# Optimization experiments

Measured on AMD Instinct MI355X. Metric: run time of the kernel, lower is better.

The kernel has to match this reference:

```python
import jax, jax.numpy as jnp
import numpy as np

H = 16      # attention_head_num
DH = 64     # attention_head_size
D = H * DH  # out_dim = 1024


def setup_inputs() -> dict:
    key = jax.random.key(0)
    ks = jax.random.split(key, 9)
    s = 1.0 / np.sqrt(D)
    x = jax.random.normal(ks[0], (2, 2048, D), dtype=jnp.float32)
    Wq = jax.random.uniform(ks[1], (D, D), jnp.float32, -s, s)
    bq = jax.random.uniform(ks[2], (D,), jnp.float32, -s, s)
    Wk = jax.random.uniform(ks[3], (D, D), jnp.float32, -s, s)
    bk = jax.random.uniform(ks[4], (D,), jnp.float32, -s, s)
    Wv = jax.random.uniform(ks[5], (D, D), jnp.float32, -s, s)
    bv = jax.random.uniform(ks[6], (D,), jnp.float32, -s, s)
    Wo = jax.random.uniform(ks[7], (D, D), jnp.float32, -s, s)
    bo = jax.random.uniform(ks[8], (D,), jnp.float32, -s, s)
    return {"x": x, "Wq": Wq, "bq": bq, "Wk": Wk, "bk": bk,
            "Wv": Wv, "bv": bv, "Wo": Wo, "bo": bo}


def reference(x, Wq, bq, Wk, bk, Wv, bv, Wo, bo):
    B, S, _ = x.shape
    # projections (nn.Linear: x @ W^T + b)
    q = (x @ Wq.T + bq).reshape(B, S, H, DH).transpose(0, 2, 1, 3)  # [B,H,S,Dh]
    k = (x @ Wk.T + bk).reshape(B, S, H, DH).transpose(0, 2, 1, 3)
    v = (x @ Wv.T + bv).reshape(B, S, H, DH).transpose(0, 2, 1, 3)
    scores = jnp.einsum('bhqd,bhkd->bhqk', q, k) / jnp.sqrt(jnp.float32(DH))
    probs = jax.nn.softmax(scores, axis=-1)  # dropout is identity in eval mode
    ctx = jnp.einsum('bhqk,bhkd->bhqd', probs, v)
    ctx = ctx.transpose(0, 2, 1, 3).reshape(B, S, D)
    return ctx @ Wo.T + bo
```

## Files before the change

kernel.cpp:

```cpp
#include <hip/hip_runtime.h>
#include <hip/hip_bf16.h>
#include <stdint.h>

typedef __attribute__((ext_vector_type(8))) short bf16x8;
typedef __attribute__((ext_vector_type(8))) unsigned short u16x8;
typedef __attribute__((ext_vector_type(4))) unsigned short u16x4;
typedef __attribute__((ext_vector_type(4))) float f32x4;

constexpr int NB  = 2;
constexpr int NS  = 2048;
constexpr int NH  = 16;
constexpr int NDH = 64;
constexpr int ND  = 1024;

static __device__ __forceinline__ unsigned short bfbits(float f) {
    union { float f; uint32_t u; } v; v.f = f;
    uint32_t u = v.u + 0x7FFFu + ((v.u >> 16) & 1u);
    return (unsigned short)(u >> 16);
}

static __device__ __forceinline__ float fexp2(float x) {
#if __has_builtin(__builtin_amdgcn_exp2f)
    return __builtin_amdgcn_exp2f(x);
#else
    return exp2f(x);
#endif
}

static __device__ __forceinline__ void gl_lds16(const void* g, void* l) {
    __builtin_amdgcn_global_load_lds(
        (const __attribute__((address_space(1))) unsigned int*)g,
        (__attribute__((address_space(3))) unsigned int*)l, 16, 0, 0);
}

__global__ __launch_bounds__(256)
void cvt_kernel(const float* __restrict__ x,  const float* __restrict__ wq,
                const float* __restrict__ wk, const float* __restrict__ wv,
                const float* __restrict__ wo,
                unsigned short* __restrict__ xb,  unsigned short* __restrict__ wqb,
                unsigned short* __restrict__ wkb, unsigned short* __restrict__ wvb,
                unsigned short* __restrict__ wob)
{
    const int b = blockIdx.x;
    const float* s; unsigned short* d; int off;
    if      (b < 2048) { s = x;  d = xb;  off = b; }
    else if (b < 2560) { s = wq; d = wqb; off = b - 2048; }
    else if (b < 3072) { s = wk; d = wkb; off = b - 2560; }
    else if (b < 3584) { s = wv; d = wvb; off = b - 3072; }
    else               { s = wo; d = wob; off = b - 3584; }
    const size_t idx = ((size_t)off * 256 + threadIdx.x) * 8;
    float4 f0 = *(const float4*)&s[idx];
    float4 f1 = *(const float4*)&s[idx + 4];
    u16x8 o;
    o[0] = bfbits(f0.x); o[1] = bfbits(f0.y); o[2] = bfbits(f0.z); o[3] = bfbits(f0.w);
    o[4] = bfbits(f1.x); o[5] = bfbits(f1.y); o[6] = bfbits(f1.z); o[7] = bfbits(f1.w);
    *(u16x8*)&d[idx] = o;
}

__global__ __launch_bounds__(256, 2)
void qkv_kernel(const unsigned short* __restrict__ xb,
                const unsigned short* __restrict__ wqb,
                const unsigned short* __restrict__ wkb,
                const unsigned short* __restrict__ wvb,
                const float* __restrict__ bq, const float* __restrict__ bk,
                const float* __restrict__ bv,
                unsigned short* __restrict__ qbuf,
                unsigned short* __restrict__ kbuf,
                unsigned short* __restrict__ vtbuf)
{
    __shared__ unsigned short As[128 * 64];
    __shared__ unsigned short Bs[128 * 64];
    __shared__ unsigned short Tt[128][136];

    const int fid = blockIdx.x + blockIdx.y * 24;
    const int xcd = fid & 7, idx = fid >> 3;
    const int bx  = idx >> 2;
    const int by  = xcd * 4 + (idx & 3);

    const int m0  = by * 128;
    const int jg0 = bx * 128;
    const int proj = jg0 >> 10;
    const int n0   = jg0 & 1023;
    const unsigned short* W = (proj == 0) ? wqb : (proj == 1) ? wkb : wvb;
    const float* bias       = (proj == 0) ? bq  : (proj == 1) ? bk  : bv;

    const int tid = threadIdx.x, lane = tid & 63, wid = tid >> 6;
    const int wm = wid >> 1, wn = wid & 1;
    const int l15 = lane & 15, g = lane >> 4;

    const f32x4 fzero = {0.f, 0.f, 0.f, 0.f};
    f32x4 acc[4][4];
#pragma unroll
    for (int i = 0; i < 4; i++)
#pragma unroll
        for (int j = 0; j < 4; j++) acc[i][j] = fzero;

    const int srow = tid >> 3;
    const int scb  = ((tid & 7) * 16) ^ ((srow & 7) << 4);
    const char* asrc = (const char*)xb + (size_t)(m0 + srow) * 2048 + scb;
    const char* bsrc = (const char*)W  + (size_t)(n0 + srow) * 2048 + scb;
    char* adst = (char*)As + tid * 16;
    char* bdst = (char*)Bs + tid * 16;
    const int xm = (l15 & 7) << 4;

    for (int k0 = 0; k0 < 1024; k0 += 64) {
#pragma unroll
        for (int i = 0; i < 4; i++) {
            gl_lds16(asrc + (size_t)i * 32 * 2048 + k0 * 2, adst + i * 4096);
            gl_lds16(bsrc + (size_t)i * 32 * 2048 + k0 * 2, bdst + i * 4096);
        }
        __syncthreads();
#pragma unroll
        for (int kk = 0; kk < 2; kk++) {
            bf16x8 af[4], bfr[4];
#pragma unroll
            for (int i = 0; i < 4; i++) {
                const int row = wm * 64 + i * 16 + l15;
                af[i] = *(const bf16x8*)((const char*)As + row * 128 + ((kk * 64 + g * 16) ^ xm));
            }
#pragma unroll
            for (int j = 0; j < 4; j++) {
                const int row = wn * 64 + j * 16 + l15;
                bfr[j] = *(const bf16x8*)((const char*)Bs + row * 128 + ((kk * 64 + g * 16) ^ xm));
            }
#pragma unroll
            for (int i = 0; i < 4; i++)
#pragma unroll
                for (int j = 0; j < 4; j++)
                    acc[i][j] = __builtin_amdgcn_mfma_f32_16x16x32_bf16(af[i], bfr[j], acc[i][j], 0, 0, 0);
        }
        __syncthreads();
    }

    if (proj < 2) {
        unsigned short* qk_out = (proj == 0) ? qbuf : kbuf;
        const float qs = (proj == 0) ? 0.18033688f : 1.0f;
#pragma unroll
        for (int j = 0; j < 4; j++) {
            const int col = n0 + wn * 64 + j * 16 + l15;
            const float bsv = bias[col];
            const int h = col >> 6, dh = col & 63;
#pragma unroll
            for (int i = 0; i < 4; i++)
#pragma unroll
                for (int r = 0; r < 4; r++) {
                    const int row = m0 + wm * 64 + i * 16 + g * 4 + r;
                    const int b_ = row >> 11, s_ = row & (NS - 1);
                    qk_out[((size_t)((b_ * NH + h) * NS + s_)) * NDH + dh] =
                        bfbits((acc[i][j][r] + bsv) * qs);
                }
        }
    } else {
#pragma unroll
        for (int j = 0; j < 4; j++) {
            const int cl = wn * 64 + j * 16 + l15;
            const float bsv = bias[n0 + cl];
#pragma unroll
            for (int i = 0; i < 4; i++) {
                u16x4 w4;
#pragma unroll
                for (int r = 0; r < 4; r++) w4[r] = bfbits(acc[i][j][r] + bsv);
                *(u16x4*)&Tt[cl][wm * 64 + i * 16 + g * 4] = w4;
            }
        }
        __syncthreads();
        const int b_ = m0 >> 11, s0 = m0 & (NS - 1);
        const int h0 = n0 >> 6;
#pragma unroll
        for (int it = 0; it < 8; it++) {
            const int c = wid * 32 + it * 4 + g;
            u16x8 v8 = *(const u16x8*)&Tt[c][l15 * 8];
            const size_t row = (size_t)(b_ * NH + h0 + (c >> 6)) * NDH + (c & 63);
            *(u16x8*)&vtbuf[row * NS + s0 + l15 * 8] = v8;
        }
    }
}

__global__ __launch_bounds__(512, 4)
void attn_kernel(const unsigned short* __restrict__ qbuf,
                 const unsigned short* __restrict__ kbuf,
                 const unsigned short* __restrict__ vtbuf,
                 unsigned short* __restrict__ ctxbuf)
{
    __shared__ unsigned short Ks[2][128 * 64];
    __shared__ unsigned short Vs[2][64 * 128];

    const int fid  = blockIdx.x + blockIdx.y * 16;
    const int nid  = (fid % 8) * 64 + fid / 8;
    const int bx   = nid % 16, bh = nid / 16;
    const int q0   = bx * 128;

    const int tid = threadIdx.x, lane = tid & 63, wid = tid >> 6;
    const int l15 = lane & 15, g = lane >> 4;

    const unsigned short* qb = qbuf  + (size_t)bh * NS * NDH;
    const unsigned short* kb = kbuf  + (size_t)bh * NS * NDH;
    const unsigned short* vb = vtbuf + (size_t)bh * NDH * NS;

    const int qrow = q0 + wid * 16 + l15;
    const bf16x8 qf0 = *(const bf16x8*)&qb[(size_t)qrow * NDH + g * 8];
    const bf16x8 qf1 = *(const bf16x8*)&qb[(size_t)qrow * NDH + 32 + g * 8];

    const short oneb = (short)0x3F80;
    const bf16x8 ones = {oneb, oneb, oneb, oneb, oneb, oneb, oneb, oneb};

    const f32x4 fzero = {0.f, 0.f, 0.f, 0.f};
    f32x4 acc[4];
#pragma unroll
    for (int d = 0; d < 4; d++) acc[d] = fzero;
    f32x4 acc_l = fzero;

    const int o = tid * 16;
    const int srow = o >> 7;
    const int scb  = (o & 127) ^ ((srow & 7) << 4);
    const char* ksrc = (const char*)kb + srow * 128 + scb;
    const char* vsrc = (const char*)vb + (size_t)srow * (NS * 2) + scb;
    char* kbase = (char*)Ks;
    char* vbase = (char*)Vs;
    const int xm = (l15 & 7) << 4;

    auto STAGE = [&](int b, int t_) {
        gl_lds16(ksrc + (size_t)t_ * 16384,        kbase + b * 16384 + o);
        gl_lds16(ksrc + (size_t)t_ * 16384 + 8192, kbase + b * 16384 + 8192 + o);
        gl_lds16(vsrc + (size_t)t_ * 256,          vbase + b * 16384 + o);
        gl_lds16(vsrc + (size_t)t_ * 256 + 128,    vbase + b * 16384 + 8192 + o);
    };

    auto QK = [&](int b, int h, f32x4 (&sv)[4]) {
        const char* ksb = kbase + b * 16384 + h * 8192;
#pragma unroll
        for (int kt = 0; kt < 4; kt++) {
            const char* rb = ksb + (kt * 16 + l15) * 128;
            bf16x8 kf0 = *(const bf16x8*)(rb + ((g * 16) ^ xm));
            bf16x8 kf1 = *(const bf16x8*)(rb + ((64 + g * 16) ^ xm));
            f32x4 s4 = fzero;
            s4 = __builtin_amdgcn_mfma_f32_16x16x32_bf16(kf0, qf0, s4, 0, 0, 0);
            s4 = __builtin_amdgcn_mfma_f32_16x16x32_bf16(kf1, qf1, s4, 0, 0, 0);
            sv[kt] = s4;
        }
    };

    auto SMPV = [&](int b, int h, f32x4 (&sv)[4]) {
        const char* vsb = vbase + b * 16384 + h * 8192;
#pragma unroll
        for (int kt = 0; kt < 4; kt++)
#pragma unroll
            for (int r = 0; r < 4; r++)
                sv[kt][r] = fexp2(sv[kt][r]);

        bf16x8 pf[2];
#pragma unroll
        for (int f = 0; f < 2; f++) {
            const int kt0 = f * 2;
            union { __hip_bfloat162 h2; uint32_t u; } c0, c1, c2, c3;
            float2 p01 = { sv[kt0][0], sv[kt0][1] };
            float2 p23 = { sv[kt0][2], sv[kt0][3] };
            float2 p45 = { sv[kt0 + 1][0], sv[kt0 + 1][1] };
            float2 p67 = { sv[kt0 + 1][2], sv[kt0 + 1][3] };
            c0.h2 = __float22bfloat162_rn(p01);
            c1.h2 = __float22bfloat162_rn(p23);
            c2.h2 = __float22bfloat162_rn(p45);
            c3.h2 = __float22bfloat162_rn(p67);
            uint32_t a0 = c0.u, a1 = c1.u, b0 = c2.u, b1 = c3.u;
            asm("v_permlane32_swap_b32 %0, %1" : "+v"(a0), "+v"(b0));
            asm("v_permlane32_swap_b32 %0, %1" : "+v"(a1), "+v"(b1));
            asm("v_permlane16_swap_b32 %0, %1" : "+v"(a0), "+v"(b0));
            asm("v_permlane16_swap_b32 %0, %1" : "+v"(a1), "+v"(b1));
            union { uint32_t w[4]; bf16x8 fr; } r_;
            r_.w[0] = a0; r_.w[1] = a1; r_.w[2] = b0; r_.w[3] = b1;
            pf[f] = r_.fr;
        }

        acc_l = __builtin_amdgcn_mfma_f32_16x16x32_bf16(pf[0], ones, acc_l, 0, 0, 0);
        acc_l = __builtin_amdgcn_mfma_f32_16x16x32_bf16(pf[1], ones, acc_l, 0, 0, 0);
#pragma unroll
        for (int d = 0; d < 4; d++) {
            const char* rb = vsb + (d * 16 + l15) * 128;
            bf16x8 vf0 = *(const bf16x8*)(rb + ((g * 16) ^ xm));
            bf16x8 vf1 = *(const bf16x8*)(rb + ((64 + g * 16) ^ xm));
            acc[d] = __builtin_amdgcn_mfma_f32_16x16x32_bf16(pf[0], vf0, acc[d], 0, 0, 0);
            acc[d] = __builtin_amdgcn_mfma_f32_16x16x32_bf16(pf[1], vf1, acc[d], 0, 0, 0);
        }
    };

    f32x4 svA[4], svB[4];

    STAGE(0, 0);
    asm volatile("s_waitcnt vmcnt(0)" ::: "memory");
    __builtin_amdgcn_s_barrier();
    asm volatile("" ::: "memory");
    QK(0, 0, svA);

    for (int t = 0; t < 15; t++) {
        const int cb = t & 1, nb = cb ^ 1;
        STAGE(nb, t + 1);
        QK(cb, 1, svB);
        SMPV(cb, 0, svA);
        SMPV(cb, 1, svB);
        asm volatile("s_waitcnt vmcnt(0)" ::: "memory");
        __builtin_amdgcn_s_barrier();
        asm volatile("" ::: "memory");
        QK(nb, 0, svA);
    }
    QK(1, 1, svB);
    SMPV(1, 0, svA);
    SMPV(1, 1, svB);

    const int b_ = bh >> 4, h_ = bh & 15;
#pragma unroll
    for (int r = 0; r < 4; r++) {
        const float inv = 1.f / acc_l[r];
        const int sq = q0 + wid * 16 + g * 4 + r;
        const size_t base = ((size_t)(b_ * NS + sq)) * ND + h_ * NDH;
#pragma unroll
        for (int d = 0; d < 4; d++)
            ctxbuf[base + d * 16 + l15] = bfbits(acc[d][r] * inv);
    }
}

__global__ __launch_bounds__(256, 2)
void out_kernel(const unsigned short* __restrict__ ctx,
                const unsigned short* __restrict__ wob,
                const float* __restrict__ bo,
                float* __restrict__ out)
{
    __shared__ unsigned short As[128 * 64];
    __shared__ unsigned short Bs[128 * 64];

    const int n0 = blockIdx.x * 128;
    const int m0 = blockIdx.y * 128;
    const int tid = threadIdx.x, lane = tid & 63, wid = tid >> 6;
    const int wm = wid >> 1, wn = wid & 1;
    const int l15 = lane & 15, g = lane >> 4;

    const f32x4 fzero = {0.f, 0.f, 0.f, 0.f};
    f32x4 acc[4][4];
#pragma unroll
    for (int i = 0; i < 4; i++)
#pragma unroll
        for (int j = 0; j < 4; j++) acc[i][j] = fzero;

    const int srow = tid >> 3;
    const int scb  = ((tid & 7) * 16) ^ ((srow & 7) << 4);
    const char* asrc = (const char*)ctx + (size_t)(m0 + srow) * 2048 + scb;
    const char* bsrc = (const char*)wob + (size_t)(n0 + srow) * 2048 + scb;
    char* adst = (char*)As + tid * 16;
    char* bdst = (char*)Bs + tid * 16;
    const int xm = (l15 & 7) << 4;

    for (int k0 = 0; k0 < 1024; k0 += 64) {
#pragma unroll
        for (int i = 0; i < 4; i++) {
            gl_lds16(asrc + (size_t)i * 32 * 2048 + k0 * 2, adst + i * 4096);
            gl_lds16(bsrc + (size_t)i * 32 * 2048 + k0 * 2, bdst + i * 4096);
        }
        __syncthreads();
#pragma unroll
        for (int kk = 0; kk < 2; kk++) {
            bf16x8 af[4], bfr[4];
#pragma unroll
            for (int i = 0; i < 4; i++) {
                const int row = wm * 64 + i * 16 + l15;
                af[i] = *(const bf16x8*)((const char*)As + row * 128 + ((kk * 64 + g * 16) ^ xm));
            }
#pragma unroll
            for (int j = 0; j < 4; j++) {
                const int row = wn * 64 + j * 16 + l15;
                bfr[j] = *(const bf16x8*)((const char*)Bs + row * 128 + ((kk * 64 + g * 16) ^ xm));
            }
#pragma unroll
            for (int i = 0; i < 4; i++)
#pragma unroll
                for (int j = 0; j < 4; j++)
                    acc[i][j] = __builtin_amdgcn_mfma_f32_16x16x32_bf16(af[i], bfr[j], acc[i][j], 0, 0, 0);
        }
        __syncthreads();
    }

#pragma unroll
    for (int j = 0; j < 4; j++) {
        const int col = n0 + wn * 64 + j * 16 + l15;
        const float bsv = bo[col];
#pragma unroll
        for (int i = 0; i < 4; i++)
#pragma unroll
            for (int r = 0; r < 4; r++) {
                const int row = m0 + wm * 64 + i * 16 + g * 4 + r;
                out[(size_t)row * ND + col] = acc[i][j][r] + bsv;
            }
    }
}

extern "C" void kernel_launch(void* const* d_in, const int* in_sizes, int n_in,
                              void* d_out, int out_size, void* d_ws, size_t ws_size,
                              hipStream_t stream) {
    const float* x  = (const float*)d_in[0];
    const float* Wq = (const float*)d_in[1];
    const float* bq = (const float*)d_in[2];
    const float* Wk = (const float*)d_in[3];
    const float* bk = (const float*)d_in[4];
    const float* Wv = (const float*)d_in[5];
    const float* bv = (const float*)d_in[6];
    const float* Wo = (const float*)d_in[7];
    const float* bo = (const float*)d_in[8];
    float* out = (float*)d_out;

    const size_t qk_elems = (size_t)NB * NH * NS * NDH;
    const size_t w_elems  = (size_t)ND * ND;
    unsigned short* qbuf   = (unsigned short*)d_ws;
    unsigned short* kbuf   = qbuf + qk_elems;
    unsigned short* vtbuf  = kbuf + qk_elems;
    unsigned short* ctxbuf = vtbuf + qk_elems;
    unsigned short* xb     = ctxbuf + qk_elems;
    unsigned short* wqb    = xb + qk_elems;
    unsigned short* wkb    = wqb + w_elems;
    unsigned short* wvb    = wkb + w_elems;
    unsigned short* wob    = wvb + w_elems;

    cvt_kernel<<<4096, 256, 0, stream>>>(x, Wq, Wk, Wv, Wo, xb, wqb, wkb, wvb, wob);
    qkv_kernel<<<dim3(24, 32), 256, 0, stream>>>(xb, wqb, wkb, wvb, bq, bk, bv,
                                                 qbuf, kbuf, vtbuf);
    attn_kernel<<<dim3(16, 32), 512, 0, stream>>>(qbuf, kbuf, vtbuf, ctxbuf);
    out_kernel<<<dim3(8, 32), 256, 0, stream>>>(ctxbuf, wob, bo, out);
}
```

Baseline: 113.5 us.

## Switch attention to 32x32x16 MFMA with 4 waves of 32 query rows

Rewrites the attention kernel to use 32x32x16 bf16 MFMA tiles. Each of 4 waves (256 threads) now owns 32 query rows instead of 8 waves owning 16 rows each. The row sum is accumulated with scalar adds plus a cross-half shuffle, replacing the ones-matrix MFMA. This is meant to raise MFMA efficiency and amortize LDS K/V fragment reads over more rows. In exchange, each wave does more serial work, uses more accumulator registers, and the per-block wave count drops.

Measured after the change: 113.8 us. About the same (+0.3%).

```diff
diff --git a/kernel.cpp b/kernel.cpp
--- a/kernel.cpp
+++ b/kernel.cpp
@@ -6,6 +6,7 @@
 typedef __attribute__((ext_vector_type(8))) unsigned short u16x8;
 typedef __attribute__((ext_vector_type(4))) unsigned short u16x4;
 typedef __attribute__((ext_vector_type(4))) float f32x4;
+typedef __attribute__((ext_vector_type(16))) float f32x16;
 
 constexpr int NB  = 2;
 constexpr int NS  = 2048;
@@ -176,7 +177,7 @@
     }
 }
 
-__global__ __launch_bounds__(512, 4)
+__global__ __launch_bounds__(256, 2)
 void attn_kernel(const unsigned short* __restrict__ qbuf,
                  const unsigned short* __restrict__ kbuf,
                  const unsigned short* __restrict__ vtbuf,
@@ -191,99 +192,113 @@
     const int q0   = bx * 128;
 
     const int tid = threadIdx.x, lane = tid & 63, wid = tid >> 6;
-    const int l15 = lane & 15, g = lane >> 4;
+    const int l31 = lane & 31, hi = lane >> 5;
 
     const unsigned short* qb = qbuf  + (size_t)bh * NS * NDH;
     const unsigned short* kb = kbuf  + (size_t)bh * NS * NDH;
     const unsigned short* vb = vtbuf + (size_t)bh * NDH * NS;
 
-    const int qrow = q0 + wid * 16 + l15;
-    const bf16x8 qf0 = *(const bf16x8*)&qb[(size_t)qrow * NDH + g * 8];
-    const bf16x8 qf1 = *(const bf16x8*)&qb[(size_t)qrow * NDH + 32 + g * 8];
-
-    const short oneb = (short)0x3F80;
-    const bf16x8 ones = {oneb, oneb, oneb, oneb, oneb, oneb, oneb, oneb};
-
-    const f32x4 fzero = {0.f, 0.f, 0.f, 0.f};
-    f32x4 acc[4];
-#pragma unroll
-    for (int d = 0; d < 4; d++) acc[d] = fzero;
-    f32x4 acc_l = fzero;
-
-    const int o = tid * 16;
-    const int srow = o >> 7;
-    const int scb  = (o & 127) ^ ((srow & 7) << 4);
-    const char* ksrc = (const char*)kb + srow * 128 + scb;
-    const char* vsrc = (const char*)vb + (size_t)srow * (NS * 2) + scb;
+    const int qrow = q0 + wid * 32 + l31;
+    bf16x8 qf[4];
+#pragma unroll
+    for (int dq = 0; dq < 4; dq++)
+        qf[dq] = *(const bf16x8*)&qb[(size_t)qrow * NDH + dq * 16 + hi * 8];
+
+    f32x16 z16 = {0.f,0.f,0.f,0.f,0.f,0.f,0.f,0.f,0.f,0.f,0.f,0.f,0.f,0.f,0.f,0.f};
+    f32x16 cacc[2];
+    cacc[0] = z16; cacc[1] = z16;
+    float l_run = 0.f;
+
     char* kbase = (char*)Ks;
     char* vbase = (char*)Vs;
-    const int xm = (l15 & 7) << 4;
 
     auto STAGE = [&](int b, int t_) {
-        gl_lds16(ksrc + (size_t)t_ * 16384,        kbase + b * 16384 + o);
-        gl_lds16(ksrc + (size_t)t_ * 16384 + 8192, kbase + b * 16384 + 8192 + o);
-        gl_lds16(vsrc + (size_t)t_ * 256,          vbase + b * 16384 + o);
-        gl_lds16(vsrc + (size_t)t_ * 256 + 128,    vbase + b * 16384 + 8192 + o);
+#pragma unroll
+        for (int c = 0; c < 4; c++) {
+            const int oc = c * 4096 + tid * 16;
+            const int kr = oc >> 7, kc = oc & 127;
+            const char* ks = (const char*)kb + (size_t)t_ * 16384 + kr * 128
+                             + (kc ^ ((kr & 7) << 4));
+            gl_lds16(ks, kbase + b * 16384 + oc);
+        }
+#pragma unroll
+        for (int c = 0; c < 4; c++) {
+            const int oc = c * 4096 + tid * 16;
+            const int sub = oc >> 13, ow = oc & 8191;
+            const int dh = ow >> 7, kc = ow & 127;
+            const char* vs = (const char*)vb + (size_t)dh * (NS * 2) + t_ * 256
+                             + sub * 128 + (kc ^ ((dh & 7) << 4));
+            gl_lds16(vs, vbase + b * 16384 + oc);
+        }
     };
 
-    auto QK = [&](int b, int h, f32x4 (&sv)[4]) {
-        const char* ksb = kbase + b * 16384 + h * 8192;
-#pragma unroll
-        for (int kt = 0; kt < 4; kt++) {
-            const char* rb = ksb + (kt * 16 + l15) * 128;
-            bf16x8 kf0 = *(const bf16x8*)(rb + ((g * 16) ^ xm));
-            bf16x8 kf1 = *(const bf16x8*)(rb + ((64 + g * 16) ^ xm));
-            f32x4 s4 = fzero;
-            s4 = __builtin_amdgcn_mfma_f32_16x16x32_bf16(kf0, qf0, s4, 0, 0, 0);
-            s4 = __builtin_amdgcn_mfma_f32_16x16x32_bf16(kf1, qf1, s4, 0, 0, 0);
-            sv[kt] = s4;
+    auto QK = [&](int b, int h, f32x16 (&sv)[2]) {
+        const char* ksb = kbase + b * 16384;
+#pragma unroll
+        for (int kb2 = 0; kb2 < 2; kb2++) {
+            const int key = h * 64 + kb2 * 32 + l31;
+            const char* rb = ksb + key * 128;
+            f32x16 s = z16;
+#pragma unroll
+            for (int dq = 0; dq < 4; dq++) {
+                bf16x8 kf = *(const bf16x8*)(rb + ((dq * 32 + hi * 16) ^ ((key & 7) << 4)));
+                s = __builtin_amdgcn_mfma_f32_32x32x16_bf16(kf, qf[dq], s, 0, 0, 0);
+            }
+            sv[kb2] = s;
         }
     };
 
-    auto SMPV = [&](int b, int h, f32x4 (&sv)[4]) {
-        const char* vsb = vbase + b * 16384 + h * 8192;
-#pragma unroll
-        for (int kt = 0; kt < 4; kt++)
-#pragma unroll
-            for (int r = 0; r < 4; r++)
-                sv[kt][r] = fexp2(sv[kt][r]);
-
-        bf16x8 pf[2];
-#pragma unroll
-        for (int f = 0; f < 2; f++) {
-            const int kt0 = f * 2;
-            union { __hip_bfloat162 h2; uint32_t u; } c0, c1, c2, c3;
-            float2 p01 = { sv[kt0][0], sv[kt0][1] };
-            float2 p23 = { sv[kt0][2], sv[kt0][3] };
-            float2 p45 = { sv[kt0 + 1][0], sv[kt0 + 1][1] };
-            float2 p67 = { sv[kt0 + 1][2], sv[kt0 + 1][3] };
-            c0.h2 = __float22bfloat162_rn(p01);
-            c1.h2 = __float22bfloat162_rn(p23);
-            c2.h2 = __float22bfloat162_rn(p45);
-            c3.h2 = __float22bfloat162_rn(p67);
-            uint32_t a0 = c0.u, a1 = c1.u, b0 = c2.u, b1 = c3.u;
-            asm("v_permlane32_swap_b32 %0, %1" : "+v"(a0), "+v"(b0));
-            asm("v_permlane32_swap_b32 %0, %1" : "+v"(a1), "+v"(b1));
-            asm("v_permlane16_swap_b32 %0, %1" : "+v"(a0), "+v"(b0));
-            asm("v_permlane16_swap_b32 %0, %1" : "+v"(a1), "+v"(b1));
-            union { uint32_t w[4]; bf16x8 fr; } r_;
-            r_.w[0] = a0; r_.w[1] = a1; r_.w[2] = b0; r_.w[3] = b1;
-            pf[f] = r_.fr;
-        }
-
-        acc_l = __builtin_amdgcn_mfma_f32_16x16x32_bf16(pf[0], ones, acc_l, 0, 0, 0);
-        acc_l = __builtin_amdgcn_mfma_f32_16x16x32_bf16(pf[1], ones, acc_l, 0, 0, 0);
-#pragma unroll
-        for (int d = 0; d < 4; d++) {
-            const char* rb = vsb + (d * 16 + l15) * 128;
-            bf16x8 vf0 = *(const bf16x8*)(rb + ((g * 16) ^ xm));
-            bf16x8 vf1 = *(const bf16x8*)(rb + ((64 + g * 16) ^ xm));
-            acc[d] = __builtin_amdgcn_mfma_f32_16x16x32_bf16(pf[0], vf0, acc[d], 0, 0, 0);
-            acc[d] = __builtin_amdgcn_mfma_f32_16x16x32_bf16(pf[1], vf1, acc[d], 0, 0, 0);
+    auto SMPV = [&](int b, int h, f32x16 (&sv)[2]) {
+        const char* vsb = vbase + b * 16384;
+        float ls = 0.f;
+#pragma unroll
+        for (int kb2 = 0; kb2 < 2; kb2++)
+#pragma unroll
+            for (int r = 0; r < 16; r++) {
+                sv[kb2][r] = fexp2(sv[kb2][r]);
+                ls += sv[kb2][r];
+            }
+        l_run += ls;
+
+        bf16x8 pa[4];
+#pragma unroll
+        for (int kb2 = 0; kb2 < 2; kb2++) {
+            uint32_t w0, w1, w2, w3, w4, w5, w6, w7;
+            union { __hip_bfloat162 h2; uint32_t u; } cc;
+            float2 p;
+            p.x = sv[kb2][0];  p.y = sv[kb2][1];  cc.h2 = __float22bfloat162_rn(p); w0 = cc.u;
+            p.x = sv[kb2][2];  p.y = sv[kb2][3];  cc.h2 = __float22bfloat162_rn(p); w1 = cc.u;
+            p.x = sv[kb2][4];  p.y = sv[kb2][5];  cc.h2 = __float22bfloat162_rn(p); w2 = cc.u;
+            p.x = sv[kb2][6];  p.y = sv[kb2][7];  cc.h2 = __float22bfloat162_rn(p); w3 = cc.u;
+            p.x = sv[kb2][8];  p.y = sv[kb2][9];  cc.h2 = __float22bfloat162_rn(p); w4 = cc.u;
+            p.x = sv[kb2][10]; p.y = sv[kb2][11]; cc.h2 = __float22bfloat162_rn(p); w5 = cc.u;
+            p.x = sv[kb2][12]; p.y = sv[kb2][13]; cc.h2 = __float22bfloat162_rn(p); w6 = cc.u;
+            p.x = sv[kb2][14]; p.y = sv[kb2][15]; cc.h2 = __float22bfloat162_rn(p); w7 = cc.u;
+            asm("v_permlane32_swap_b32 %0, %1" : "+v"(w0), "+v"(w2));
+            asm("v_permlane32_swap_b32 %0, %1" : "+v"(w1), "+v"(w3));
+            asm("v_permlane32_swap_b32 %0, %1" : "+v"(w4), "+v"(w6));
+            asm("v_permlane32_swap_b32 %0, %1" : "+v"(w5), "+v"(w7));
+            union { uint32_t u[4]; bf16x8 fr; } f0, f1;
+            f0.u[0] = w0; f0.u[1] = w1; f0.u[2] = w2; f0.u[3] = w3;
+            f1.u[0] = w4; f1.u[1] = w5; f1.u[2] = w6; f1.u[3] = w7;
+            pa[kb2 * 2 + 0] = f0.fr;
+            pa[kb2 * 2 + 1] = f1.fr;
+        }
+
+#pragma unroll
+        for (int j = 0; j < 4; j++) {
+            const int kcb = (j & 3) * 32 + hi * 16;
+#pragma unroll
+            for (int dhh = 0; dhh < 2; dhh++) {
+                const int row = dhh * 32 + l31;
+                const char* rb = vsb + h * 8192 + row * 128 + (kcb ^ ((row & 7) << 4));
+                bf16x8 vf = *(const bf16x8*)rb;
+                cacc[dhh] = __builtin_amdgcn_mfma_f32_32x32x16_bf16(pa[j], vf, cacc[dhh], 0, 0, 0);
+            }
         }
     };
 
-    f32x4 svA[4], svB[4];
+    f32x16 svA[2], svB[2];
 
     STAGE(0, 0);
     asm volatile("s_waitcnt vmcnt(0)" ::: "memory");
@@ -306,15 +321,17 @@
     SMPV(1, 0, svA);
     SMPV(1, 1, svB);
 
+    const float lt = l_run + __shfl_xor(l_run, 32);
     const int b_ = bh >> 4, h_ = bh & 15;
 #pragma unroll
-    for (int r = 0; r < 4; r++) {
-        const float inv = 1.f / acc_l[r];
-        const int sq = q0 + wid * 16 + g * 4 + r;
+    for (int r = 0; r < 16; r++) {
+        const int ql = (r & 3) + 8 * (r >> 2) + 4 * hi;
+        const float lq = __shfl(lt, ql);
+        const float inv = 1.f / lq;
+        const int sq = q0 + wid * 32 + ql;
         const size_t base = ((size_t)(b_ * NS + sq)) * ND + h_ * NDH;
-#pragma unroll
-        for (int d = 0; d < 4; d++)
-            ctxbuf[base + d * 16 + l15] = bfbits(acc[d][r] * inv);
+        ctxbuf[base + l31]      = bfbits(cacc[0][r] * inv);
+        ctxbuf[base + 32 + l31] = bfbits(cacc[1][r] * inv);
     }
 }
 
@@ -420,6 +437,6 @@
     cvt_kernel<<<4096, 256, 0, stream>>>(x, Wq, Wk, Wv, Wo, xb, wqb, wkb, wvb, wob);
     qkv_kernel<<<dim3(24, 32), 256, 0, stream>>>(xb, wqb, wkb, wvb, bq, bk, bv,
                                                  qbuf, kbuf, vtbuf);
-    attn_kernel<<<dim3(16, 32), 512, 0, stream>>>(qbuf, kbuf, vtbuf, ctxbuf);
+    attn_kernel<<<dim3(16, 32), 256, 0, stream>>>(qbuf, kbuf, vtbuf, ctxbuf);
     out_kernel<<<dim3(8, 32), 256, 0, stream>>>(ctxbuf, wob, bo, out);
 }
```
